# Kernel optimization log

Measured on AMD Instinct MI355X. Metric: run time of the kernel, lower is better.

## Reference

```python
import jax, jax.numpy as jnp
import numpy as np

NUM_ITERS = 3
EPS = 1e-8
LN_EPS = 1e-5


def _ln(x, g, b):
    m = x.mean(-1, keepdims=True)
    v = ((x - m) ** 2).mean(-1, keepdims=True)
    return (x - m) * jax.lax.rsqrt(v + LN_EPS) * g + b


def setup_inputs() -> dict:
    key = jax.random.key(0)
    ks = jax.random.split(key, 20)
    B, S, N, C = 32, 16, 16384, 128
    H = C  # hidden_dim defaults to dim
    s = 0.02
    f32 = jnp.float32
    return {
        "slots": jax.random.normal(ks[0], (B, S, C), f32),
        "inputs": jax.random.normal(ks[1], (B, N, C), f32),
        # projections (stored [in,out]; y = x @ W)
        "Wq": jax.random.normal(ks[2], (C, C), f32) * s,
        "Wk": jax.random.normal(ks[3], (C, C), f32) * s,
        "Wv": jax.random.normal(ks[4], (C, C), f32) * s,
        # GRUCell params, gate order r,z,n (stored [in, 3C])
        "gru_wih": jax.random.normal(ks[5], (C, 3 * C), f32) * s,
        "gru_whh": jax.random.normal(ks[6], (C, 3 * C), f32) * s,
        "gru_bih": jnp.zeros((3 * C,), f32),
        "gru_bhh": jnp.zeros((3 * C,), f32),
        # MLP
        "mlp_w1": jax.random.normal(ks[7], (C, H), f32) * s,
        "mlp_b1": jnp.zeros((H,), f32),
        "mlp_w2": jax.random.normal(ks[8], (H, C), f32) * s,
        "mlp_b2": jnp.zeros((C,), f32),
        # LayerNorms
        "ln_in_g": jnp.ones((C,), f32),
        "ln_in_b": jnp.zeros((C,), f32),
        "ln_s_g": jnp.ones((C,), f32),
        "ln_s_b": jnp.zeros((C,), f32),
        "ln_ff_g": jnp.ones((C,), f32),
        "ln_ff_b": jnp.zeros((C,), f32),
    }


def reference(slots, inputs, Wq, Wk, Wv, gru_wih, gru_whh, gru_bih, gru_bhh,
              mlp_w1, mlp_b1, mlp_w2, mlp_b2,
              ln_in_g, ln_in_b, ln_s_g, ln_s_b, ln_ff_g, ln_ff_b):
    B, S, C = slots.shape
    scale = np.sqrt(C)
    x = _ln(inputs, ln_in_g, ln_in_b)          # pos_embed = Identity
    k = x @ Wk                                  # [B,N,C]
    v = x @ Wv                                  # [B,N,C]
    for _ in range(NUM_ITERS):
        slots_prev = slots
        q = (_ln(slots, ln_s_g, ln_s_b) @ Wq) / scale      # [B,S,C]
        dots = jnp.einsum('bqd,bkd->bqk', q, k)            # [B,S,N]
        attn = jax.nn.softmax(dots, axis=-2) + EPS         # softmax over slots
        attn = attn / attn.sum(-1, keepdims=True)          # renorm over keys
        updates = jnp.einsum('bkd,bqk->bqd', v, attn)      # [B,S,C]
        # GRUCell (torch semantics, gates r,z,n)
        gi = updates @ gru_wih + gru_bih
        gh = slots_prev @ gru_whh + gru_bhh
        ir, iz, in_ = jnp.split(gi, 3, axis=-1)
        hr, hz, hn = jnp.split(gh, 3, axis=-1)
        r = jax.nn.sigmoid(ir + hr)
        z = jax.nn.sigmoid(iz + hz)
        n = jnp.tanh(in_ + r * hn)
        slots = (1.0 - z) * n + z * slots_prev
        # residual MLP
        h = jax.nn.relu(_ln(slots, ln_ff_g, ln_ff_b) @ mlp_w1 + mlp_b1)
        slots = slots + (h @ mlp_w2 + mlp_b2)
    return slots
```

## Files before the change

kernel.cpp:

```cpp
#include <hip/hip_runtime.h>


#define NTOT 16384
#define CDIM 128

using short8 = __attribute__((ext_vector_type(8))) short;
using f32x4  = __attribute__((ext_vector_type(4))) float;
using u32x2  = __attribute__((ext_vector_type(2))) unsigned;

__device__ __forceinline__ unsigned pkbf(float lo, float hi) {
  unsigned r;
  asm("v_cvt_pk_bf16_f32 %0, %1, %2" : "=v"(r) : "v"(lo), "v"(hi));
  return r;
}
__device__ __forceinline__ float sigf(float x) { return 1.f / (1.f + __expf(-x)); }
__device__ __forceinline__ float tanhfast(float x) {
  x = fminf(fmaxf(x, -15.f), 15.f);
  float e = __expf(2.f * x);
  return (e - 1.f) / (e + 1.f);
}

__global__ __launch_bounds__(256) void k0_wqk(const float* __restrict__ Wq,
    const float* __restrict__ Wk, float* __restrict__ wqk) {
  int idx = blockIdx.x * 256 + threadIdx.x;
  int cq = idx >> 7, ck = idx & 127;
  const float* a = Wq + cq * 128;
  const float* b = Wk + ck * 128;
  float s = 0.f;
  #pragma unroll 8
  for (int i = 0; i < 128; i += 4) {
    f32x4 av = *(const f32x4*)(a + i), bv = *(const f32x4*)(b + i);
    s += av[0]*bv[0] + av[1]*bv[1] + av[2]*bv[2] + av[3]*bv[3];
  }
  wqk[idx] = s;
}

__global__ __launch_bounds__(256) void k1_ln(const float* __restrict__ in,
    const float* __restrict__ gam, const float* __restrict__ bet,
    unsigned short* __restrict__ xln) {
  __shared__ __align__(16) unsigned short xb[64 * 136];
  __shared__ float gs[128], bs[128];
  const int t = threadIdx.x, w = t >> 6, l = t & 63, lr = l & 15, lg = l >> 4;
  if (t < 128) { gs[t] = gam[t]; bs[t] = bet[t]; }
  const long rowbase = (long)blockIdx.x * 64;
  const float* src = in + (rowbase + w * 16 + lr) * CDIM;
  f32x4 x[4][2];
  #pragma unroll
  for (int kb = 0; kb < 4; ++kb) {
    x[kb][0] = *(const f32x4*)(src + kb * 32 + lg * 8);
    x[kb][1] = *(const f32x4*)(src + kb * 32 + lg * 8 + 4);
  }
  float s1 = 0.f, s2 = 0.f;
  #pragma unroll
  for (int kb = 0; kb < 4; ++kb)
    #pragma unroll
    for (int h = 0; h < 2; ++h)
      #pragma unroll
      for (int i = 0; i < 4; ++i) { float xx = x[kb][h][i]; s1 += xx; s2 += xx * xx; }
  s1 += __shfl_xor(s1, 16); s1 += __shfl_xor(s1, 32);
  s2 += __shfl_xor(s2, 16); s2 += __shfl_xor(s2, 32);
  const float mean = s1 * (1.f / 128.f);
  const float rstd = rsqrtf(s2 * (1.f / 128.f) - mean * mean + 1e-5f);
  __syncthreads();
  #pragma unroll
  for (int kb = 0; kb < 4; ++kb) {
    int c0 = kb * 32 + lg * 8;
    union { unsigned uw[4]; short8 s8; } cv;
    #pragma unroll
    for (int p = 0; p < 2; ++p) {
      float y0 = (x[kb][p][0] - mean) * rstd * gs[c0 + p*4 + 0] + bs[c0 + p*4 + 0];
      float y1 = (x[kb][p][1] - mean) * rstd * gs[c0 + p*4 + 1] + bs[c0 + p*4 + 1];
      float y2 = (x[kb][p][2] - mean) * rstd * gs[c0 + p*4 + 2] + bs[c0 + p*4 + 2];
      float y3 = (x[kb][p][3] - mean) * rstd * gs[c0 + p*4 + 3] + bs[c0 + p*4 + 3];
      cv.uw[p*2 + 0] = pkbf(y0, y1);
      cv.uw[p*2 + 1] = pkbf(y2, y3);
    }
    *(short8*)(xb + (w * 16 + lr) * 136 + c0) = cv.s8;
  }
  asm volatile("" ::: "memory");
  unsigned short* dst = xln + (rowbase + w * 16) * CDIM;
  #pragma unroll
  for (int i = 0; i < 4; ++i) {
    int row = i * 4 + (l >> 4), cb = (l & 15) * 8;
    short8 v = *(const short8*)(xb + (w * 16 + row) * 136 + cb);
    *(short8*)(dst + row * CDIM + cb) = v;
  }
}

__global__ __launch_bounds__(512) void kq_init(
    const float* __restrict__ slots, const float* __restrict__ lnsg,
    const float* __restrict__ lnsb, const float* __restrict__ wqk,
    unsigned short* __restrict__ qout) {
  const int b = blockIdx.x, t = threadIdx.x;
  const int s = t >> 5, jq = (t & 31) * 4;
  __shared__ __align__(16) float lnq[2048];
  f32x4 x4 = *(const f32x4*)(slots + b * 2048 + t * 4);
  float ps = x4[0] + x4[1] + x4[2] + x4[3];
  float pq = x4[0]*x4[0] + x4[1]*x4[1] + x4[2]*x4[2] + x4[3]*x4[3];
  ps += __shfl_xor(ps, 1); ps += __shfl_xor(ps, 2); ps += __shfl_xor(ps, 4); ps += __shfl_xor(ps, 8); ps += __shfl_xor(ps, 16);
  pq += __shfl_xor(pq, 1); pq += __shfl_xor(pq, 2); pq += __shfl_xor(pq, 4); pq += __shfl_xor(pq, 8); pq += __shfl_xor(pq, 16);
  float mean = ps * (1.f / 128.f);
  float var  = pq * (1.f / 128.f) - mean * mean;
  float rstd = rsqrtf(var + 1e-5f);
  f32x4 l4 = (x4 - mean) * rstd * (*(const f32x4*)(lnsg + jq)) + (*(const f32x4*)(lnsb + jq));
  *(f32x4*)(lnq + t * 4) = l4;
  __syncthreads();
  f32x4 qa = {0.f, 0.f, 0.f, 0.f};
  const float* wqp = wqk + jq;
  const float* qrow = lnq + s * 128;
  for (int c = 0; c < 128; ++c)
    qa += *(const f32x4*)(wqp + c * 128) * qrow[c];
  qa *= 0.08838834764831845f;
  u32x2 pk = { pkbf(qa[0], qa[1]), pkbf(qa[2], qa[3]) };
  *(u32x2*)(qout + b * 2048 + t * 4) = pk;
}

__global__ __launch_bounds__(256) void k2_attn(
    const unsigned short* __restrict__ xln, const unsigned short* __restrict__ qm,
    float* __restrict__ nump, float* __restrict__ denp) {
  const int nb = blockIdx.x, b = blockIdx.y;
  const int t = threadIdx.x, w = t >> 6, l = t & 63, lr = l & 15, lg = l >> 4;
  __shared__ __align__(16) unsigned short xT[4][4096];
  __shared__ __align__(16) unsigned short pbuf[4][16*40];

  const unsigned short* xb = xln + (long)b * (NTOT * CDIM);
  const unsigned short* qb = qm + b * 2048;

  short8 qf[4];
  #pragma unroll
  for (int kk = 0; kk < 4; ++kk)
    qf[kk] = *(const short8*)(qb + lr * CDIM + kk * 32 + lg * 8);

  f32x4 acc[8];
  #pragma unroll
  for (int i = 0; i < 8; ++i) acc[i] = (f32x4){0.f, 0.f, 0.f, 0.f};
  f32x4 dacc = {0.f, 0.f, 0.f, 0.f};

  const int base_n = nb * 512 + w * 32;
  char* xTc = (char*)&xT[w][0];
  unsigned short* pbw = &pbuf[w][0];
  const unsigned swz_rd = (((unsigned)lr >> 1) & 3u) << 4;

  short8 xk[2][8];
  #pragma unroll
  for (int h = 0; h < 2; ++h)
    #pragma unroll
    for (int kk = 0; kk < 4; ++kk)
      xk[0][h*4+kk] = *(const short8*)(xb + (long)(base_n + h*16 + lr) * CDIM + kk*32 + lg*8);

  #pragma unroll
  for (int it = 0; it < 4; ++it) {
    if (it < 3) {
      const int n1 = base_n + (it + 1) * 128;
      #pragma unroll
      for (int h = 0; h < 2; ++h)
        #pragma unroll
        for (int kk = 0; kk < 4; ++kk)
          xk[(it+1)&1][h*4+kk] = *(const short8*)(xb + (long)(n1 + h*16 + lr) * CDIM + kk*32 + lg*8);
    }
    #pragma unroll
    for (int r = 0; r < 8; ++r) {
      const int h = r >> 2, kk = r & 3;
      const unsigned wb = (unsigned)(kk * 2048 + lg * 512 + (h * 16 + lr) * 2);
      #pragma unroll
      for (int e = 0; e < 8; ++e) {
        unsigned off = (wb + e * 64) ^ ((((unsigned)e >> 1) & 3u) << 4);
        *(unsigned short*)(xTc + off) = (unsigned short)xk[it&1][r][e];
      }
    }
    #pragma unroll
    for (int h = 0; h < 2; ++h) {
      f32x4 d = {0.f, 0.f, 0.f, 0.f};
      #pragma unroll
      for (int kk = 0; kk < 4; ++kk)
        d = __builtin_amdgcn_mfma_f32_16x16x32_bf16(qf[kk], xk[it&1][h*4+kk], d, 0, 0, 0);
      float e0 = __expf(d[0]), e1 = __expf(d[1]), e2 = __expf(d[2]), e3 = __expf(d[3]);
      float cs = e0 + e1 + e2 + e3;
      cs += __shfl_xor(cs, 16);
      cs += __shfl_xor(cs, 32);
      float inv = 1.f / cs;
      float p0 = e0 * inv + 1e-8f, p1 = e1 * inv + 1e-8f,
            p2 = e2 * inv + 1e-8f, p3 = e3 * inv + 1e-8f;
      dacc[0] += p0; dacc[1] += p1; dacc[2] += p2; dacc[3] += p3;
      unsigned w01 = pkbf(p0, p1), w23 = pkbf(p2, p3);
      const int nn = h * 16 + lr;
      pbw[(lg*4 + 0) * 40 + nn] = (unsigned short)w01;
      pbw[(lg*4 + 1) * 40 + nn] = (unsigned short)(w01 >> 16);
      pbw[(lg*4 + 2) * 40 + nn] = (unsigned short)w23;
      pbw[(lg*4 + 3) * 40 + nn] = (unsigned short)(w23 >> 16);
    }
    asm volatile("" ::: "memory");
    short8 pf = *(const short8*)(pbw + lr * 40 + lg * 8);
    #pragma unroll
    for (int ct = 0; ct < 8; ++ct) {
      unsigned off = ((unsigned)((ct*16 + lr) * 64 + lg * 16)) ^ swz_rd;
      short8 af = *(const short8*)(xTc + off);
      acc[ct] = __builtin_amdgcn_mfma_f32_16x16x32_bf16(af, pf, acc[ct], 0, 0, 0);
    }
    asm volatile("" ::: "memory");
  }

  #pragma unroll
  for (int m = 1; m <= 8; m <<= 1) {
    dacc[0] += __shfl_xor(dacc[0], m); dacc[1] += __shfl_xor(dacc[1], m);
    dacc[2] += __shfl_xor(dacc[2], m); dacc[3] += __shfl_xor(dacc[3], m);
  }
  float* outp = nump + (((long)b * 32 + nb) * 4 + w) * 2048;
  #pragma unroll
  for (int ct = 0; ct < 8; ++ct)
    *(f32x4*)(outp + lr * 128 + ct * 16 + lg * 4) = acc[ct];
  if (lr == 0) {
    #pragma unroll
    for (int r = 0; r < 4; ++r)
      denp[(((long)b * 32 + nb) * 4 + w) * 16 + lg * 4 + r] = dacc[r];
  }
}

__global__ __launch_bounds__(128) void k3_update(
    const float* __restrict__ sprev, const float* __restrict__ nump,
    const float* __restrict__ denp, const float* __restrict__ Wv,
    const float* __restrict__ wih, const float* __restrict__ whh,
    const float* __restrict__ bih, const float* __restrict__ bhh,
    const float* __restrict__ w1, const float* __restrict__ b1,
    const float* __restrict__ w2, const float* __restrict__ b2,
    const float* __restrict__ lnfg, const float* __restrict__ lnfb,
    const float* __restrict__ lnsg, const float* __restrict__ lnsb,
    const float* __restrict__ wqk,
    float* __restrict__ sout, unsigned short* __restrict__ qout, const int doq) {
  const int g = blockIdx.x, b = blockIdx.y, t = threadIdx.x;
  const int sl = t >> 5, jq = (t & 31) * 4;
  const int s = g * 4 + sl;
  const long base = (long)b * 2048 + g * 512;
  __shared__ __align__(16) float sp[512];
  __shared__ __align__(16) float upd[512];
  __shared__ __align__(16) float upd2[512];
  __shared__ __align__(16) float lnb[512];
  __shared__ __align__(16) float denred[2][4];

  f32x4 dv = *(const f32x4*)(denp + ((long)b * 128 + t) * 16 + g * 4);
  #pragma unroll
  for (int m = 1; m <= 32; m <<= 1) {
    dv[0] += __shfl_xor(dv[0], m); dv[1] += __shfl_xor(dv[1], m);
    dv[2] += __shfl_xor(dv[2], m); dv[3] += __shfl_xor(dv[3], m);
  }
  if ((t & 63) == 0) *(f32x4*)denred[t >> 6] = dv;

  f32x4 hp4 = *(const f32x4*)(sprev + base + t * 4);
  *(f32x4*)(sp + t * 4) = hp4;

  f32x4 ns = {0.f, 0.f, 0.f, 0.f};
  const float* np = nump + (long)b * 262144 + s * 128 + jq;
  #pragma unroll 4
  for (int p = 0; p < 128; ++p) ns += *(const f32x4*)(np + (long)p * 2048);
  __syncthreads();
  float den_s = denred[0][sl] + denred[1][sl];
  *(f32x4*)(upd + t * 4) = ns * (1.f / den_s);
  __syncthreads();

  f32x4 ud = {0,0,0,0};
  const float* nxr = upd + sl * 128;
  for (int c = 0; c < 128; ++c)
    ud += *(const f32x4*)(Wv + c * 128 + jq) * nxr[c];
  *(f32x4*)(upd2 + t * 4) = ud;
  __syncthreads();

  f32x4 ir = {0,0,0,0}, iz = {0,0,0,0}, inn = {0,0,0,0};
  f32x4 hr = {0,0,0,0}, hz = {0,0,0,0}, hn = {0,0,0,0};
  const float* wih_p = wih + jq;
  const float* whh_p = whh + jq;
  const float* ur  = upd2 + sl * 128;
  const float* hrw = sp + sl * 128;
  for (int c = 0; c < 128; ++c) {
    float u = ur[c], h = hrw[c];
    ir  += *(const f32x4*)(wih_p + c * 384)       * u;
    iz  += *(const f32x4*)(wih_p + c * 384 + 128) * u;
    inn += *(const f32x4*)(wih_p + c * 384 + 256) * u;
    hr  += *(const f32x4*)(whh_p + c * 384)       * h;
    hz  += *(const f32x4*)(whh_p + c * 384 + 128) * h;
    hn  += *(const f32x4*)(whh_p + c * 384 + 256) * h;
  }
  ir  += *(const f32x4*)(bih + jq);
  iz  += *(const f32x4*)(bih + 128 + jq);
  inn += *(const f32x4*)(bih + 256 + jq);
  hr  += *(const f32x4*)(bhh + jq);
  hz  += *(const f32x4*)(bhh + 128 + jq);
  hn  += *(const f32x4*)(bhh + 256 + jq);
  f32x4 snew;
  #pragma unroll
  for (int i = 0; i < 4; ++i) {
    float r = sigf(ir[i] + hr[i]);
    float z = sigf(iz[i] + hz[i]);
    float n = tanhfast(inn[i] + r * hn[i]);
    snew[i] = (1.f - z) * n + z * hp4[i];
  }

  float ps = snew[0] + snew[1] + snew[2] + snew[3];
  float pq = snew[0]*snew[0] + snew[1]*snew[1] + snew[2]*snew[2] + snew[3]*snew[3];
  ps += __shfl_xor(ps, 1); ps += __shfl_xor(ps, 2); ps += __shfl_xor(ps, 4); ps += __shfl_xor(ps, 8); ps += __shfl_xor(ps, 16);
  pq += __shfl_xor(pq, 1); pq += __shfl_xor(pq, 2); pq += __shfl_xor(pq, 4); pq += __shfl_xor(pq, 8); pq += __shfl_xor(pq, 16);
  float mean = ps * (1.f / 128.f);
  float var  = pq * (1.f / 128.f) - mean * mean;
  float rstd = rsqrtf(var + 1e-5f);
  f32x4 lf = (snew - mean) * rstd * (*(const f32x4*)(lnfg + jq)) + (*(const f32x4*)(lnfb + jq));
  *(f32x4*)(lnb + t * 4) = lf;
  __syncthreads();

  f32x4 ha = {0,0,0,0};
  const float* w1p = w1 + jq;
  const float* lrow = lnb + sl * 128;
  for (int c = 0; c < 128; ++c)
    ha += *(const f32x4*)(w1p + c * 128) * lrow[c];
  ha += *(const f32x4*)(b1 + jq);
  #pragma unroll
  for (int i = 0; i < 4; ++i) ha[i] = fmaxf(ha[i], 0.f);
  *(f32x4*)(upd + t * 4) = ha;
  __syncthreads();

  f32x4 oa = {0,0,0,0};
  const float* w2p = w2 + jq;
  const float* hrow = upd + sl * 128;
  for (int c = 0; c < 128; ++c)
    oa += *(const f32x4*)(w2p + c * 128) * hrow[c];
  oa += *(const f32x4*)(b2 + jq);
  f32x4 sf = snew + oa;
  *(f32x4*)(sout + base + t * 4) = sf;

  if (doq) {
    float qs = sf[0] + sf[1] + sf[2] + sf[3];
    float qz = sf[0]*sf[0] + sf[1]*sf[1] + sf[2]*sf[2] + sf[3]*sf[3];
    qs += __shfl_xor(qs, 1); qs += __shfl_xor(qs, 2); qs += __shfl_xor(qs, 4); qs += __shfl_xor(qs, 8); qs += __shfl_xor(qs, 16);
    qz += __shfl_xor(qz, 1); qz += __shfl_xor(qz, 2); qz += __shfl_xor(qz, 4); qz += __shfl_xor(qz, 8); qz += __shfl_xor(qz, 16);
    float m2 = qs * (1.f / 128.f);
    float v2 = qz * (1.f / 128.f) - m2 * m2;
    float rs2 = rsqrtf(v2 + 1e-5f);
    f32x4 lq = (sf - m2) * rs2 * (*(const f32x4*)(lnsg + jq)) + (*(const f32x4*)(lnsb + jq));
    *(f32x4*)(sp + t * 4) = lq;
    __syncthreads();
    f32x4 qa = {0,0,0,0};
    const float* wqp = wqk + jq;
    const float* qrow = sp + sl * 128;
    for (int c = 0; c < 128; ++c)
      qa += *(const f32x4*)(wqp + c * 128) * qrow[c];
    qa *= 0.08838834764831845f;
    u32x2 pk = { pkbf(qa[0], qa[1]), pkbf(qa[2], qa[3]) };
    *(u32x2*)(qout + base + t * 4) = pk;
  }
}

extern "C" void kernel_launch(void* const* d_in, const int* in_sizes, int n_in,
                              void* d_out, int out_size, void* d_ws, size_t ws_size,
                              hipStream_t stream) {
  (void)in_sizes; (void)n_in; (void)out_size; (void)ws_size;
  const float* slots = (const float*)d_in[0];
  const float* inputs = (const float*)d_in[1];
  const float* Wq  = (const float*)d_in[2];
  const float* Wk  = (const float*)d_in[3];
  const float* Wv  = (const float*)d_in[4];
  const float* wih = (const float*)d_in[5];
  const float* whh = (const float*)d_in[6];
  const float* bih = (const float*)d_in[7];
  const float* bhh = (const float*)d_in[8];
  const float* w1  = (const float*)d_in[9];
  const float* b1  = (const float*)d_in[10];
  const float* w2  = (const float*)d_in[11];
  const float* b2  = (const float*)d_in[12];
  const float* lnig = (const float*)d_in[13];
  const float* lnib = (const float*)d_in[14];
  const float* lnsg = (const float*)d_in[15];
  const float* lnsb = (const float*)d_in[16];
  const float* lnfg = (const float*)d_in[17];
  const float* lnfb = (const float*)d_in[18];

  char* ws = (char*)d_ws;
  unsigned short* xln  = (unsigned short*)(ws);
  unsigned short* qbuf = (unsigned short*)(ws + 134217728L);
  float* wqk  = (float*)(ws + 134348800L);
  float* nump = (float*)(ws + 134414336L);
  float* denp = (float*)(ws + 167968768L);
  float* sbuf = (float*)(ws + 168230912L);

  k0_wqk<<<64, 256, 0, stream>>>(Wq, Wk, wqk);
  k1_ln<<<8192, 256, 0, stream>>>(inputs, lnig, lnib, xln);
  kq_init<<<32, 512, 0, stream>>>(slots, lnsg, lnsb, wqk, qbuf);
  for (int it = 0; it < 3; ++it) {
    k2_attn<<<dim3(32, 32), 256, 0, stream>>>(xln, qbuf, nump, denp);
    const float* sprev = (it == 0) ? slots : sbuf;
    float* sdst = (it == 2) ? (float*)d_out : sbuf;
    k3_update<<<dim3(4, 32), 128, 0, stream>>>(sprev, nump, denp, Wv,
                                      wih, whh, bih, bhh, w1, b1, w2, b2,
                                      lnfg, lnfb, lnsg, lnsb, wqk,
                                      sdst, qbuf, (it < 2) ? 1 : 0);
  }
}
```

Before: 368.0 us.

## Fuse input LayerNorm into first attention pass and reduce partial outputs in-block

Removes the separate LayerNorm kernel and the Wq·Wk precompute kernel. The first attention launch now reads fp32 inputs, normalizes them in registers, uses them directly and writes the bf16 copy for later iterations. Query projection is computed as two chained matvecs on Wq and Wk. Attention blocks reduce the partial numerators of four waves to two in shared memory, which halves the partial buffer traffic read by the update kernel. The LDS transpose swizzle also changes to avoid bank conflicts. In exchange, the first attention pass loses its prefetch pipelining, and the query step does more arithmetic.

```diff
diff --git a/kernel.cpp b/kernel.cpp
--- a/kernel.cpp
+++ b/kernel.cpp
@@ -20,80 +20,14 @@
   return (e - 1.f) / (e + 1.f);
 }
 
-__global__ __launch_bounds__(256) void k0_wqk(const float* __restrict__ Wq,
-    const float* __restrict__ Wk, float* __restrict__ wqk) {
-  int idx = blockIdx.x * 256 + threadIdx.x;
-  int cq = idx >> 7, ck = idx & 127;
-  const float* a = Wq + cq * 128;
-  const float* b = Wk + ck * 128;
-  float s = 0.f;
-  #pragma unroll 8
-  for (int i = 0; i < 128; i += 4) {
-    f32x4 av = *(const f32x4*)(a + i), bv = *(const f32x4*)(b + i);
-    s += av[0]*bv[0] + av[1]*bv[1] + av[2]*bv[2] + av[3]*bv[3];
-  }
-  wqk[idx] = s;
-}
-
-__global__ __launch_bounds__(256) void k1_ln(const float* __restrict__ in,
-    const float* __restrict__ gam, const float* __restrict__ bet,
-    unsigned short* __restrict__ xln) {
-  __shared__ __align__(16) unsigned short xb[64 * 136];
-  __shared__ float gs[128], bs[128];
-  const int t = threadIdx.x, w = t >> 6, l = t & 63, lr = l & 15, lg = l >> 4;
-  if (t < 128) { gs[t] = gam[t]; bs[t] = bet[t]; }
-  const long rowbase = (long)blockIdx.x * 64;
-  const float* src = in + (rowbase + w * 16 + lr) * CDIM;
-  f32x4 x[4][2];
-  #pragma unroll
-  for (int kb = 0; kb < 4; ++kb) {
-    x[kb][0] = *(const f32x4*)(src + kb * 32 + lg * 8);
-    x[kb][1] = *(const f32x4*)(src + kb * 32 + lg * 8 + 4);
-  }
-  float s1 = 0.f, s2 = 0.f;
-  #pragma unroll
-  for (int kb = 0; kb < 4; ++kb)
-    #pragma unroll
-    for (int h = 0; h < 2; ++h)
-      #pragma unroll
-      for (int i = 0; i < 4; ++i) { float xx = x[kb][h][i]; s1 += xx; s2 += xx * xx; }
-  s1 += __shfl_xor(s1, 16); s1 += __shfl_xor(s1, 32);
-  s2 += __shfl_xor(s2, 16); s2 += __shfl_xor(s2, 32);
-  const float mean = s1 * (1.f / 128.f);
-  const float rstd = rsqrtf(s2 * (1.f / 128.f) - mean * mean + 1e-5f);
-  __syncthreads();
-  #pragma unroll
-  for (int kb = 0; kb < 4; ++kb) {
-    int c0 = kb * 32 + lg * 8;
-    union { unsigned uw[4]; short8 s8; } cv;
-    #pragma unroll
-    for (int p = 0; p < 2; ++p) {
-      float y0 = (x[kb][p][0] - mean) * rstd * gs[c0 + p*4 + 0] + bs[c0 + p*4 + 0];
-      float y1 = (x[kb][p][1] - mean) * rstd * gs[c0 + p*4 + 1] + bs[c0 + p*4 + 1];
-      float y2 = (x[kb][p][2] - mean) * rstd * gs[c0 + p*4 + 2] + bs[c0 + p*4 + 2];
-      float y3 = (x[kb][p][3] - mean) * rstd * gs[c0 + p*4 + 3] + bs[c0 + p*4 + 3];
-      cv.uw[p*2 + 0] = pkbf(y0, y1);
-      cv.uw[p*2 + 1] = pkbf(y2, y3);
-    }
-    *(short8*)(xb + (w * 16 + lr) * 136 + c0) = cv.s8;
-  }
-  asm volatile("" ::: "memory");
-  unsigned short* dst = xln + (rowbase + w * 16) * CDIM;
-  #pragma unroll
-  for (int i = 0; i < 4; ++i) {
-    int row = i * 4 + (l >> 4), cb = (l & 15) * 8;
-    short8 v = *(const short8*)(xb + (w * 16 + row) * 136 + cb);
-    *(short8*)(dst + row * CDIM + cb) = v;
-  }
-}
-
 __global__ __launch_bounds__(512) void kq_init(
     const float* __restrict__ slots, const float* __restrict__ lnsg,
-    const float* __restrict__ lnsb, const float* __restrict__ wqk,
-    unsigned short* __restrict__ qout) {
+    const float* __restrict__ lnsb, const float* __restrict__ Wq,
+    const float* __restrict__ Wk, unsigned short* __restrict__ qout) {
   const int b = blockIdx.x, t = threadIdx.x;
   const int s = t >> 5, jq = (t & 31) * 4;
   __shared__ __align__(16) float lnq[2048];
+  __shared__ __align__(16) float q1b[2048];
   f32x4 x4 = *(const f32x4*)(slots + b * 2048 + t * 4);
   float ps = x4[0] + x4[1] + x4[2] + x4[3];
   float pq = x4[0]*x4[0] + x4[1]*x4[1] + x4[2]*x4[2] + x4[3]*x4[3];
@@ -105,25 +39,47 @@
   f32x4 l4 = (x4 - mean) * rstd * (*(const f32x4*)(lnsg + jq)) + (*(const f32x4*)(lnsb + jq));
   *(f32x4*)(lnq + t * 4) = l4;
   __syncthreads();
-  f32x4 qa = {0.f, 0.f, 0.f, 0.f};
-  const float* wqp = wqk + jq;
+  f32x4 q1 = {0.f, 0.f, 0.f, 0.f};
   const float* qrow = lnq + s * 128;
   for (int c = 0; c < 128; ++c)
-    qa += *(const f32x4*)(wqp + c * 128) * qrow[c];
+    q1 += *(const f32x4*)(Wq + c * 128 + jq) * qrow[c];
+  *(f32x4*)(q1b + t * 4) = q1;
+  __syncthreads();
+  const float* q1r = q1b + s * 128;
+  f32x4 qa = {0.f, 0.f, 0.f, 0.f};
+  for (int c2 = 0; c2 < 128; c2 += 4) {
+    f32x4 qv = *(const f32x4*)(q1r + c2);
+    #pragma unroll
+    for (int i = 0; i < 4; ++i) {
+      f32x4 wv = *(const f32x4*)(Wk + (jq + i) * 128 + c2);
+      qa[i] += qv[0]*wv[0] + qv[1]*wv[1] + qv[2]*wv[2] + qv[3]*wv[3];
+    }
+  }
   qa *= 0.08838834764831845f;
   u32x2 pk = { pkbf(qa[0], qa[1]), pkbf(qa[2], qa[3]) };
   *(u32x2*)(qout + b * 2048 + t * 4) = pk;
 }
 
-__global__ __launch_bounds__(256) void k2_attn(
-    const unsigned short* __restrict__ xln, const unsigned short* __restrict__ qm,
+template<int DOLN>
+__global__ __launch_bounds__(256, 4) void k2_attn(
+    const float* __restrict__ inputs, const float* __restrict__ gam,
+    const float* __restrict__ bet, unsigned short* __restrict__ xln,
+    const unsigned short* __restrict__ qm,
     float* __restrict__ nump, float* __restrict__ denp) {
   const int nb = blockIdx.x, b = blockIdx.y;
   const int t = threadIdx.x, w = t >> 6, l = t & 63, lr = l & 15, lg = l >> 4;
-  __shared__ __align__(16) unsigned short xT[4][4096];
-  __shared__ __align__(16) unsigned short pbuf[4][16*40];
-
-  const unsigned short* xb = xln + (long)b * (NTOT * CDIM);
+  __shared__ __align__(16) char smem[38912];
+  char* xTc = smem + w * 8192;
+  unsigned short* pbw = (unsigned short*)(smem + 32768) + w * 640;
+  float* gs = (float*)(smem + 37888);
+  float* bs = gs + 128;
+
+  if (DOLN) {
+    if (t < 128) { gs[t] = gam[t]; bs[t] = bet[t]; }
+    __syncthreads();
+  }
+
+  unsigned short* xb = xln + (long)b * (NTOT * CDIM);
   const unsigned short* qb = qm + b * 2048;
 
   short8 qf[4];
@@ -137,35 +93,80 @@
   f32x4 dacc = {0.f, 0.f, 0.f, 0.f};
 
   const int base_n = nb * 512 + w * 32;
-  char* xTc = (char*)&xT[w][0];
-  unsigned short* pbw = &pbuf[w][0];
-  const unsigned swz_rd = (((unsigned)lr >> 1) & 3u) << 4;
-
-  short8 xk[2][8];
-  #pragma unroll
-  for (int h = 0; h < 2; ++h)
-    #pragma unroll
-    for (int kk = 0; kk < 4; ++kk)
-      xk[0][h*4+kk] = *(const short8*)(xb + (long)(base_n + h*16 + lr) * CDIM + kk*32 + lg*8);
-
-  #pragma unroll
-  for (int it = 0; it < 4; ++it) {
-    if (it < 3) {
-      const int n1 = base_n + (it + 1) * 128;
-      #pragma unroll
-      for (int h = 0; h < 2; ++h)
+
+  short8 xnext[8];
+  if (!DOLN) {
+    #pragma unroll
+    for (int h = 0; h < 2; ++h)
+      #pragma unroll
+      for (int kk = 0; kk < 4; ++kk)
+        xnext[h*4+kk] = *(const short8*)(xb + (long)(base_n + h*16 + lr) * CDIM + kk*32 + lg*8);
+  }
+
+  #pragma unroll
+  for (int itt = 0; itt < 4; ++itt) {
+    const int n0 = base_n + itt * 128;
+    short8 xcur[8];
+    if (DOLN) {
+      #pragma unroll
+      for (int h = 0; h < 2; ++h) {
+        const float* src = inputs + ((long)b * NTOT + n0 + h * 16 + lr) * CDIM + lg * 8;
+        f32x4 xx[4][2];
+        #pragma unroll
+        for (int kk = 0; kk < 4; ++kk) {
+          xx[kk][0] = *(const f32x4*)(src + kk * 32);
+          xx[kk][1] = *(const f32x4*)(src + kk * 32 + 4);
+        }
+        float s1 = 0.f, s2 = 0.f;
         #pragma unroll
         for (int kk = 0; kk < 4; ++kk)
-          xk[(it+1)&1][h*4+kk] = *(const short8*)(xb + (long)(n1 + h*16 + lr) * CDIM + kk*32 + lg*8);
-    }
+          #pragma unroll
+          for (int p = 0; p < 2; ++p)
+            #pragma unroll
+            for (int i = 0; i < 4; ++i) { float v = xx[kk][p][i]; s1 += v; s2 += v * v; }
+        s1 += __shfl_xor(s1, 16); s1 += __shfl_xor(s1, 32);
+        s2 += __shfl_xor(s2, 16); s2 += __shfl_xor(s2, 32);
+        const float mean = s1 * (1.f / 128.f);
+        const float rstd = rsqrtf(s2 * (1.f / 128.f) - mean * mean + 1e-5f);
+        #pragma unroll
+        for (int kk = 0; kk < 4; ++kk) {
+          int c0 = kk * 32 + lg * 8;
+          union { unsigned uw[4]; short8 s8; } cv;
+          #pragma unroll
+          for (int p = 0; p < 2; ++p) {
+            float y0 = (xx[kk][p][0] - mean) * rstd * gs[c0 + p*4 + 0] + bs[c0 + p*4 + 0];
+            float y1 = (xx[kk][p][1] - mean) * rstd * gs[c0 + p*4 + 1] + bs[c0 + p*4 + 1];
+            float y2 = (xx[kk][p][2] - mean) * rstd * gs[c0 + p*4 + 2] + bs[c0 + p*4 + 2];
+            float y3 = (xx[kk][p][3] - mean) * rstd * gs[c0 + p*4 + 3] + bs[c0 + p*4 + 3];
+            cv.uw[p*2 + 0] = pkbf(y0, y1);
+            cv.uw[p*2 + 1] = pkbf(y2, y3);
+          }
+          xcur[h*4+kk] = cv.s8;
+          *(short8*)(xb + (long)(n0 + h*16 + lr) * CDIM + c0) = cv.s8;
+        }
+      }
+    } else {
+      #pragma unroll
+      for (int r = 0; r < 8; ++r) xcur[r] = xnext[r];
+      if (itt < 3) {
+        const int n1 = base_n + (itt + 1) * 128;
+        #pragma unroll
+        for (int h = 0; h < 2; ++h)
+          #pragma unroll
+          for (int kk = 0; kk < 4; ++kk)
+            xnext[h*4+kk] = *(const short8*)(xb + (long)(n1 + h*16 + lr) * CDIM + kk*32 + lg*8);
+      }
+    }
+
     #pragma unroll
     for (int r = 0; r < 8; ++r) {
       const int h = r >> 2, kk = r & 3;
       const unsigned wb = (unsigned)(kk * 2048 + lg * 512 + (h * 16 + lr) * 2);
       #pragma unroll
       for (int e = 0; e < 8; ++e) {
-        unsigned off = (wb + e * 64) ^ ((((unsigned)e >> 1) & 3u) << 4);
-        *(unsigned short*)(xTc + off) = (unsigned short)xk[it&1][r][e];
+        unsigned key = ((((unsigned)e >> 1) & 3u) ^ (unsigned)lg) << 4;
+        unsigned off = (wb + e * 64) ^ key;
+        *(unsigned short*)(xTc + off) = (unsigned short)xcur[r][e];
       }
     }
     #pragma unroll
@@ -173,7 +174,7 @@
       f32x4 d = {0.f, 0.f, 0.f, 0.f};
       #pragma unroll
       for (int kk = 0; kk < 4; ++kk)
-        d = __builtin_amdgcn_mfma_f32_16x16x32_bf16(qf[kk], xk[it&1][h*4+kk], d, 0, 0, 0);
+        d = __builtin_amdgcn_mfma_f32_16x16x32_bf16(qf[kk], xcur[h*4+kk], d, 0, 0, 0);
       float e0 = __expf(d[0]), e1 = __expf(d[1]), e2 = __expf(d[2]), e3 = __expf(d[3]);
       float cs = e0 + e1 + e2 + e3;
       cs += __shfl_xor(cs, 16);
@@ -193,7 +194,9 @@
     short8 pf = *(const short8*)(pbw + lr * 40 + lg * 8);
     #pragma unroll
     for (int ct = 0; ct < 8; ++ct) {
-      unsigned off = ((unsigned)((ct*16 + lr) * 64 + lg * 16)) ^ swz_rd;
+      unsigned key = (((((unsigned)lr >> 1) & 3u) ^
+                      (((unsigned)(ct * 2) + ((unsigned)lr >> 3)) & 3u)) << 4);
+      unsigned off = ((unsigned)((ct*16 + lr) * 64 + lg * 16)) ^ key;
       short8 af = *(const short8*)(xTc + off);
       acc[ct] = __builtin_amdgcn_mfma_f32_16x16x32_bf16(af, pf, acc[ct], 0, 0, 0);
     }
@@ -205,14 +208,34 @@
     dacc[0] += __shfl_xor(dacc[0], m); dacc[1] += __shfl_xor(dacc[1], m);
     dacc[2] += __shfl_xor(dacc[2], m); dacc[3] += __shfl_xor(dacc[3], m);
   }
-  float* outp = nump + (((long)b * 32 + nb) * 4 + w) * 2048;
-  #pragma unroll
-  for (int ct = 0; ct < 8; ++ct)
-    *(f32x4*)(outp + lr * 128 + ct * 16 + lg * 4) = acc[ct];
-  if (lr == 0) {
-    #pragma unroll
-    for (int r = 0; r < 4; ++r)
-      denp[(((long)b * 32 + nb) * 4 + w) * 16 + lg * 4 + r] = dacc[r];
+  __syncthreads();
+  if (w >= 2) {
+    float* rb = (float*)(smem + (w - 2) * 8192);
+    #pragma unroll
+    for (int ct = 0; ct < 8; ++ct)
+      *(f32x4*)(rb + lr * 128 + ct * 16 + lg * 4) = acc[ct];
+    if (lr == 0) {
+      float* db = (float*)(smem + 32768) + (w - 2) * 16;
+      #pragma unroll
+      for (int r = 0; r < 4; ++r) db[lg * 4 + r] = dacc[r];
+    }
+  }
+  __syncthreads();
+  if (w < 2) {
+    const float* rb = (float*)(smem + w * 8192);
+    float* outp = nump + (((long)b * 32 + nb) * 2 + w) * 2048;
+    #pragma unroll
+    for (int ct = 0; ct < 8; ++ct) {
+      f32x4 other = *(const f32x4*)(rb + lr * 128 + ct * 16 + lg * 4);
+      *(f32x4*)(outp + lr * 128 + ct * 16 + lg * 4) = acc[ct] + other;
+    }
+    if (lr == 0) {
+      const float* db = (float*)(smem + 32768) + w * 16;
+      #pragma unroll
+      for (int r = 0; r < 4; ++r)
+        denp[(((long)b * 32 + nb) * 2 + w) * 16 + lg * 4 + r] =
+            dacc[r] + db[lg * 4 + r];
+    }
   }
 }
 
@@ -225,7 +248,7 @@
     const float* __restrict__ w2, const float* __restrict__ b2,
     const float* __restrict__ lnfg, const float* __restrict__ lnfb,
     const float* __restrict__ lnsg, const float* __restrict__ lnsb,
-    const float* __restrict__ wqk,
+    const float* __restrict__ Wq, const float* __restrict__ Wk,
     float* __restrict__ sout, unsigned short* __restrict__ qout, const int doq) {
   const int g = blockIdx.x, b = blockIdx.y, t = threadIdx.x;
   const int sl = t >> 5, jq = (t & 31) * 4;
@@ -235,26 +258,27 @@
   __shared__ __align__(16) float upd[512];
   __shared__ __align__(16) float upd2[512];
   __shared__ __align__(16) float lnb[512];
-  __shared__ __align__(16) float denred[2][4];
-
-  f32x4 dv = *(const f32x4*)(denp + ((long)b * 128 + t) * 16 + g * 4);
-  #pragma unroll
-  for (int m = 1; m <= 32; m <<= 1) {
-    dv[0] += __shfl_xor(dv[0], m); dv[1] += __shfl_xor(dv[1], m);
-    dv[2] += __shfl_xor(dv[2], m); dv[3] += __shfl_xor(dv[3], m);
-  }
-  if ((t & 63) == 0) *(f32x4*)denred[t >> 6] = dv;
+  __shared__ __align__(16) float denred[4];
+
+  if (t < 64) {
+    f32x4 dv = *(const f32x4*)(denp + ((long)b * 64 + t) * 16 + g * 4);
+    #pragma unroll
+    for (int m = 1; m <= 32; m <<= 1) {
+      dv[0] += __shfl_xor(dv[0], m); dv[1] += __shfl_xor(dv[1], m);
+      dv[2] += __shfl_xor(dv[2], m); dv[3] += __shfl_xor(dv[3], m);
+    }
+    if (t == 0) *(f32x4*)denred = dv;
+  }
 
   f32x4 hp4 = *(const f32x4*)(sprev + base + t * 4);
   *(f32x4*)(sp + t * 4) = hp4;
 
   f32x4 ns = {0.f, 0.f, 0.f, 0.f};
-  const float* np = nump + (long)b * 262144 + s * 128 + jq;
+  const float* np = nump + (long)b * 131072 + s * 128 + jq;
   #pragma unroll 4
-  for (int p = 0; p < 128; ++p) ns += *(const f32x4*)(np + (long)p * 2048);
-  __syncthreads();
-  float den_s = denred[0][sl] + denred[1][sl];
-  *(f32x4*)(upd + t * 4) = ns * (1.f / den_s);
+  for (int p = 0; p < 64; ++p) ns += *(const f32x4*)(np + (long)p * 2048);
+  __syncthreads();
+  *(f32x4*)(upd + t * 4) = ns * (1.f / denred[sl]);
   __syncthreads();
 
   f32x4 ud = {0,0,0,0};
@@ -336,11 +360,22 @@
     f32x4 lq = (sf - m2) * rs2 * (*(const f32x4*)(lnsg + jq)) + (*(const f32x4*)(lnsb + jq));
     *(f32x4*)(sp + t * 4) = lq;
     __syncthreads();
-    f32x4 qa = {0,0,0,0};
-    const float* wqp = wqk + jq;
+    f32x4 q1 = {0,0,0,0};
     const float* qrow = sp + sl * 128;
     for (int c = 0; c < 128; ++c)
-      qa += *(const f32x4*)(wqp + c * 128) * qrow[c];
+      q1 += *(const f32x4*)(Wq + c * 128 + jq) * qrow[c];
+    *(f32x4*)(upd2 + t * 4) = q1;
+    __syncthreads();
+    const float* q1r = upd2 + sl * 128;
+    f32x4 qa = {0,0,0,0};
+    for (int c2 = 0; c2 < 128; c2 += 4) {
+      f32x4 qv = *(const f32x4*)(q1r + c2);
+      #pragma unroll
+      for (int i = 0; i < 4; ++i) {
+        f32x4 wv = *(const f32x4*)(Wk + (jq + i) * 128 + c2);
+        qa[i] += qv[0]*wv[0] + qv[1]*wv[1] + qv[2]*wv[2] + qv[3]*wv[3];
+      }
+    }
     qa *= 0.08838834764831845f;
     u32x2 pk = { pkbf(qa[0], qa[1]), pkbf(qa[2], qa[3]) };
     *(u32x2*)(qout + base + t * 4) = pk;
@@ -374,21 +409,23 @@
   char* ws = (char*)d_ws;
   unsigned short* xln  = (unsigned short*)(ws);
   unsigned short* qbuf = (unsigned short*)(ws + 134217728L);
-  float* wqk  = (float*)(ws + 134348800L);
-  float* nump = (float*)(ws + 134414336L);
-  float* denp = (float*)(ws + 167968768L);
-  float* sbuf = (float*)(ws + 168230912L);
-
-  k0_wqk<<<64, 256, 0, stream>>>(Wq, Wk, wqk);
-  k1_ln<<<8192, 256, 0, stream>>>(inputs, lnig, lnib, xln);
-  kq_init<<<32, 512, 0, stream>>>(slots, lnsg, lnsb, wqk, qbuf);
+  float* nump = (float*)(ws + 134348800L);
+  float* denp = (float*)(ws + 151126016L);
+  float* sbuf = (float*)(ws + 151257088L);
+
+  kq_init<<<32, 512, 0, stream>>>(slots, lnsg, lnsb, Wq, Wk, qbuf);
   for (int it = 0; it < 3; ++it) {
-    k2_attn<<<dim3(32, 32), 256, 0, stream>>>(xln, qbuf, nump, denp);
+    if (it == 0)
+      k2_attn<1><<<dim3(32, 32), 256, 0, stream>>>(inputs, lnig, lnib, xln,
+                                                   qbuf, nump, denp);
+    else
+      k2_attn<0><<<dim3(32, 32), 256, 0, stream>>>(inputs, lnig, lnib, xln,
+                                                   qbuf, nump, denp);
     const float* sprev = (it == 0) ? slots : sbuf;
     float* sdst = (it == 2) ? (float*)d_out : sbuf;
     k3_update<<<dim3(4, 32), 128, 0, stream>>>(sprev, nump, denp, Wv,
                                       wih, whh, bih, bhh, w1, b1, w2, b2,
-                                      lnfg, lnfb, lnsg, lnsb, wqk,
+                                      lnfg, lnfb, lnsg, lnsb, Wq, Wk,
                                       sdst, qbuf, (it < 2) ? 1 : 0);
   }
 }
```

Result: slower. 618.3 us (+68.0%).

## Reduce attention partials in-block via LDS and fix xT swizzle bank conflicts

Applied to the files above, without the earlier changes.

The attention kernel now sums the partial numerator and denominator tiles of wave pairs in shared memory before writing to global. This halves the partial buffer size and the number of partials the update kernel must reduce. The LDS transpose swizzle key also now mixes in the lane group and tile index, to cut bank conflicts on the scatter writes and fragment reads. In exchange it adds two block barriers and reuses the xT/pbuf LDS as scratch at the end of the kernel.

```diff
diff --git a/kernel.cpp b/kernel.cpp
--- a/kernel.cpp
+++ b/kernel.cpp
@@ -139,7 +139,6 @@
   const int base_n = nb * 512 + w * 32;
   char* xTc = (char*)&xT[w][0];
   unsigned short* pbw = &pbuf[w][0];
-  const unsigned swz_rd = (((unsigned)lr >> 1) & 3u) << 4;
 
   short8 xk[2][8];
   #pragma unroll
@@ -164,7 +163,8 @@
       const unsigned wb = (unsigned)(kk * 2048 + lg * 512 + (h * 16 + lr) * 2);
       #pragma unroll
       for (int e = 0; e < 8; ++e) {
-        unsigned off = (wb + e * 64) ^ ((((unsigned)e >> 1) & 3u) << 4);
+        unsigned key = ((((unsigned)e >> 1) & 3u) ^ (unsigned)lg) << 4;
+        unsigned off = (wb + e * 64) ^ key;
         *(unsigned short*)(xTc + off) = (unsigned short)xk[it&1][r][e];
       }
     }
@@ -193,7 +193,9 @@
     short8 pf = *(const short8*)(pbw + lr * 40 + lg * 8);
     #pragma unroll
     for (int ct = 0; ct < 8; ++ct) {
-      unsigned off = ((unsigned)((ct*16 + lr) * 64 + lg * 16)) ^ swz_rd;
+      unsigned key = (((((unsigned)lr >> 1) & 3u) ^
+                      (((unsigned)(ct * 2) + ((unsigned)lr >> 3)) & 3u)) << 4);
+      unsigned off = ((unsigned)((ct*16 + lr) * 64 + lg * 16)) ^ key;
       short8 af = *(const short8*)(xTc + off);
       acc[ct] = __builtin_amdgcn_mfma_f32_16x16x32_bf16(af, pf, acc[ct], 0, 0, 0);
     }
@@ -205,14 +207,34 @@
     dacc[0] += __shfl_xor(dacc[0], m); dacc[1] += __shfl_xor(dacc[1], m);
     dacc[2] += __shfl_xor(dacc[2], m); dacc[3] += __shfl_xor(dacc[3], m);
   }
-  float* outp = nump + (((long)b * 32 + nb) * 4 + w) * 2048;
-  #pragma unroll
-  for (int ct = 0; ct < 8; ++ct)
-    *(f32x4*)(outp + lr * 128 + ct * 16 + lg * 4) = acc[ct];
-  if (lr == 0) {
-    #pragma unroll
-    for (int r = 0; r < 4; ++r)
-      denp[(((long)b * 32 + nb) * 4 + w) * 16 + lg * 4 + r] = dacc[r];
+  __syncthreads();
+  if (w >= 2) {
+    float* rb = (float*)((char*)&xT[0][0] + (w - 2) * 8192);
+    #pragma unroll
+    for (int ct = 0; ct < 8; ++ct)
+      *(f32x4*)(rb + lr * 128 + ct * 16 + lg * 4) = acc[ct];
+    if (lr == 0) {
+      float* db = (float*)&pbuf[0][0] + (w - 2) * 16;
+      #pragma unroll
+      for (int r = 0; r < 4; ++r) db[lg * 4 + r] = dacc[r];
+    }
+  }
+  __syncthreads();
+  if (w < 2) {
+    const float* rb = (float*)((char*)&xT[0][0] + w * 8192);
+    float* outp = nump + (((long)b * 32 + nb) * 2 + w) * 2048;
+    #pragma unroll
+    for (int ct = 0; ct < 8; ++ct) {
+      f32x4 other = *(const f32x4*)(rb + lr * 128 + ct * 16 + lg * 4);
+      *(f32x4*)(outp + lr * 128 + ct * 16 + lg * 4) = acc[ct] + other;
+    }
+    if (lr == 0) {
+      const float* db = (float*)&pbuf[0][0] + w * 16;
+      #pragma unroll
+      for (int r = 0; r < 4; ++r)
+        denp[(((long)b * 32 + nb) * 2 + w) * 16 + lg * 4 + r] =
+            dacc[r] + db[lg * 4 + r];
+    }
   }
 }
 
@@ -235,26 +257,27 @@
   __shared__ __align__(16) float upd[512];
   __shared__ __align__(16) float upd2[512];
   __shared__ __align__(16) float lnb[512];
-  __shared__ __align__(16) float denred[2][4];
-
-  f32x4 dv = *(const f32x4*)(denp + ((long)b * 128 + t) * 16 + g * 4);
-  #pragma unroll
-  for (int m = 1; m <= 32; m <<= 1) {
-    dv[0] += __shfl_xor(dv[0], m); dv[1] += __shfl_xor(dv[1], m);
-    dv[2] += __shfl_xor(dv[2], m); dv[3] += __shfl_xor(dv[3], m);
-  }
-  if ((t & 63) == 0) *(f32x4*)denred[t >> 6] = dv;
+  __shared__ __align__(16) float denred[4];
+
+  if (t < 64) {
+    f32x4 dv = *(const f32x4*)(denp + ((long)b * 64 + t) * 16 + g * 4);
+    #pragma unroll
+    for (int m = 1; m <= 32; m <<= 1) {
+      dv[0] += __shfl_xor(dv[0], m); dv[1] += __shfl_xor(dv[1], m);
+      dv[2] += __shfl_xor(dv[2], m); dv[3] += __shfl_xor(dv[3], m);
+    }
+    if (t == 0) *(f32x4*)denred = dv;
+  }
 
   f32x4 hp4 = *(const f32x4*)(sprev + base + t * 4);
   *(f32x4*)(sp + t * 4) = hp4;
 
   f32x4 ns = {0.f, 0.f, 0.f, 0.f};
-  const float* np = nump + (long)b * 262144 + s * 128 + jq;
+  const float* np = nump + (long)b * 131072 + s * 128 + jq;
   #pragma unroll 4
-  for (int p = 0; p < 128; ++p) ns += *(const f32x4*)(np + (long)p * 2048);
-  __syncthreads();
-  float den_s = denred[0][sl] + denred[1][sl];
-  *(f32x4*)(upd + t * 4) = ns * (1.f / den_s);
+  for (int p = 0; p < 64; ++p) ns += *(const f32x4*)(np + (long)p * 2048);
+  __syncthreads();
+  *(f32x4*)(upd + t * 4) = ns * (1.f / denred[sl]);
   __syncthreads();
 
   f32x4 ud = {0,0,0,0};
@@ -376,8 +399,8 @@
   unsigned short* qbuf = (unsigned short*)(ws + 134217728L);
   float* wqk  = (float*)(ws + 134348800L);
   float* nump = (float*)(ws + 134414336L);
-  float* denp = (float*)(ws + 167968768L);
-  float* sbuf = (float*)(ws + 168230912L);
+  float* denp = (float*)(ws + 151191552L);
+  float* sbuf = (float*)(ws + 151322624L);
 
   k0_wqk<<<64, 256, 0, stream>>>(Wq, Wk, wqk);
   k1_ln<<<8192, 256, 0, stream>>>(inputs, lnig, lnib, xln);
```

Measured after the change: 349.2 us. -5.1%, faster.
